# Optimization experiments

Hardware: AMD Instinct MI355X
Metric: run time of the kernel (lower is better)

## Reference

```python
import jax, jax.numpy as jnp
import numpy as np

N = 100000
E = 1600000
C_IN = 32
C_OUT = 64
DIM = 3
K = 2 ** DIM  # kernel_size=2 per pseudo-dim, degree=1 => 8 kernel slots
EPS = 1e-5

_BITS = jnp.asarray(np.array([[(c >> d) & 1 for d in range(DIM)] for c in range(K)], dtype=np.float32))  # [K,DIM]


def spline_basis(edge_attr):
    # edge_attr: [E,DIM] pseudo coords in [0,1]. kernel_size=2, degree=1 =>
    # per-dim linear basis (1-u, u); product over dims gives [E,K].
    u = edge_attr[:, None, :]            # [E,1,DIM]
    b = _BITS[None, :, :]                # [1,K,DIM]
    return jnp.prod(b * u + (1.0 - b) * (1.0 - u), axis=-1)  # [E,K]


def spline_conv(x, edge_index, edge_attr, W, W_root):
    # SplineConv with aggr='mean', root_weight=True, bias=False.
    src, dst = edge_index[0], edge_index[1]
    basis = spline_basis(edge_attr)                      # [E,K]
    x_j = x[src]                                         # [E,C_in] gather
    msg = jnp.einsum('ek,ei,kio->eo', basis, x_j, W)     # [E,C_out]
    agg = jax.ops.segment_sum(msg, dst, num_segments=N)  # [N,C_out] scatter-add
    cnt = jax.ops.segment_sum(jnp.ones((msg.shape[0],), msg.dtype), dst, num_segments=N)
    agg = agg / jnp.maximum(cnt, 1.0)[:, None]           # mean aggregation
    return agg + x @ W_root


def batch_norm(x, gamma, beta):
    mu = jnp.mean(x, axis=0)
    var = jnp.var(x, axis=0)
    return (x - mu) * jax.lax.rsqrt(var + EPS) * gamma + beta


def setup_inputs() -> dict:
    key = jax.random.key(0)
    ks = jax.random.split(key, 12)
    x = jax.random.normal(ks[0], (N, C_IN), jnp.float32)
    edge_index = jax.random.randint(ks[1], (2, E), 0, N, jnp.int32)
    edge_attr = jax.random.uniform(ks[2], (E, DIM), jnp.float32)
    s1 = 1.0 / np.sqrt(C_IN)
    s2 = 1.0 / np.sqrt(C_OUT)
    return {
        'x': x,
        'edge_index': edge_index,
        'edge_attr': edge_attr,
        'W1': jax.random.normal(ks[3], (K, C_IN, C_OUT), jnp.float32) * s1,
        'root1': jax.random.normal(ks[4], (C_IN, C_OUT), jnp.float32) * s1,
        'g1': jnp.ones((C_OUT,), jnp.float32),
        'b1': jnp.zeros((C_OUT,), jnp.float32),
        'W2': jax.random.normal(ks[5], (K, C_OUT, C_OUT), jnp.float32) * s2,
        'root2': jax.random.normal(ks[6], (C_OUT, C_OUT), jnp.float32) * s2,
        'g2': jnp.ones((C_OUT,), jnp.float32),
        'b2': jnp.zeros((C_OUT,), jnp.float32),
        'W_skip': jax.random.normal(ks[7], (C_IN, C_OUT), jnp.float32) * s1,
        'g_skip': jnp.ones((C_OUT,), jnp.float32),
        'b_skip': jnp.zeros((C_OUT,), jnp.float32),
    }


def reference(x, edge_index, edge_attr, W1, root1, g1, b1, W2, root2, g2, b2, W_skip, g_skip, b_skip):
    # ConvBlock: SplineConv -> BN -> elu
    h = spline_conv(x, edge_index, edge_attr, W1, root1)
    h = jax.nn.elu(batch_norm(h, g1, b1))
    # ConvBlockWithSkip: SplineConv -> BN; Linear skip -> BN; elu(sum)
    skip = batch_norm(x @ W_skip, g_skip, b_skip)
    h2 = batch_norm(spline_conv(h, edge_index, edge_attr, W2, root2), g2, b2)
    return jax.nn.elu(h2 + skip)
```

## Files before the change

kernel.cpp:

```cpp
#include <hip/hip_runtime.h>
#include <cstdint>

#define BN_EPS 1e-5f

typedef __attribute__((ext_vector_type(8))) short bf16x8;
typedef __attribute__((ext_vector_type(4))) float f32x4;
typedef __attribute__((ext_vector_type(2))) float f32x2;
typedef unsigned int uint32;
typedef unsigned short u16;

__device__ inline u16 f2bf(float f) {
  unsigned int b = __float_as_uint(f);
  b += 0x7FFFu + ((b >> 16) & 1u);
  return (u16)(b >> 16);
}
__device__ inline float bf2f(u16 u) { return __uint_as_float((unsigned int)u << 16); }

__global__ __launch_bounds__(256) void prep(const float* __restrict__ W1,
                                            const float* __restrict__ root1,
                                            const float* __restrict__ Wskip,
                                            const float* __restrict__ W2,
                                            const float* __restrict__ root2,
                                            u16* __restrict__ B1t, u16* __restrict__ B2t,
                                            const float* __restrict__ x,
                                            u16* __restrict__ xbf, int total8) {
  int idx = blockIdx.x * 256 + threadIdx.x;
  if (idx < 128 * 288) {
    int n = idx / 288, a = idx % 288;
    float v;
    if (a < 256) {
      int i = a >> 3, k = a & 7;
      v = (n < 64) ? W1[k * 2048 + i * 64 + n] : 0.f;
    } else {
      int i = a - 256;
      v = (n < 64) ? root1[i * 64 + n] : Wskip[i * 64 + (n - 64)];
    }
    B1t[idx] = f2bf(v);
  } else if (idx < 128 * 288 + 64 * 576) {
    int j = idx - 128 * 288;
    int n = j / 576, a = j % 576;
    float v;
    if (a < 512) {
      int i = a >> 3, k = a & 7;
      v = W2[k * 4096 + i * 64 + n];
    } else {
      v = root2[(a - 512) * 64 + n];
    }
    B2t[j] = f2bf(v);
  }
  if (idx < total8) {
    const float4* xp = (const float4*)x;
    float4 a = xp[2 * idx], b = xp[2 * idx + 1];
    union { u16 s[8]; uint4 u; } p;
    p.s[0] = f2bf(a.x); p.s[1] = f2bf(a.y); p.s[2] = f2bf(a.z); p.s[3] = f2bf(a.w);
    p.s[4] = f2bf(b.x); p.s[5] = f2bf(b.y); p.s[6] = f2bf(b.z); p.s[7] = f2bf(b.w);
    ((uint4*)xbf)[idx] = p.u;
  }
}

__global__ void hist_dst(const int* __restrict__ ei, int E, int* __restrict__ indeg,
                         int* __restrict__ rank) {
  int e = blockIdx.x * 256 + threadIdx.x;
  if (e >= E) return;
  rank[e] = atomicAdd(&indeg[ei[E + e]], 1);
}

__global__ __launch_bounds__(1024) void scan_block(const int* __restrict__ in,
                                                   int* __restrict__ part,
                                                   int* __restrict__ bsum, int N) {
  __shared__ int tmp[1024];
  int i = blockIdx.x * 1024 + threadIdx.x;
  int v = (i < N) ? in[i] : 0;
  tmp[threadIdx.x] = v;
  __syncthreads();
  for (int ofs = 1; ofs < 1024; ofs <<= 1) {
    int t = (threadIdx.x >= (unsigned)ofs) ? tmp[threadIdx.x - ofs] : 0;
    __syncthreads();
    tmp[threadIdx.x] += t;
    __syncthreads();
  }
  if (i < N) part[i] = tmp[threadIdx.x] - v;
  if (threadIdx.x == 1023) bsum[blockIdx.x] = tmp[1023];
}

__global__ __launch_bounds__(1024) void scan_top(int* __restrict__ bsum, int nb) {
  __shared__ int tmp[1024];
  int v = (threadIdx.x < (unsigned)nb) ? bsum[threadIdx.x] : 0;
  tmp[threadIdx.x] = v;
  __syncthreads();
  for (int ofs = 1; ofs < 1024; ofs <<= 1) {
    int t = (threadIdx.x >= (unsigned)ofs) ? tmp[threadIdx.x - ofs] : 0;
    __syncthreads();
    tmp[threadIdx.x] += t;
    __syncthreads();
  }
  if (threadIdx.x < (unsigned)nb) bsum[threadIdx.x] = tmp[threadIdx.x] - v;
}

__global__ void scan_add(const int* __restrict__ part, const int* __restrict__ bsum,
                         int* __restrict__ rowptr, int N, int E) {
  int i = blockIdx.x * 256 + threadIdx.x;
  if (i < N) rowptr[i] = part[i] + bsum[i >> 10];
  if (i == 0) rowptr[N] = E;
}

__global__ __launch_bounds__(256) void edge_scatter(const int* __restrict__ ei,
                                                    const float* __restrict__ attr,
                                                    const int* __restrict__ rowptr,
                                                    const int* __restrict__ rank, int E,
                                                    uint4* __restrict__ emeta) {
  int e = blockIdx.x * 256 + threadIdx.x;
  if (e >= E) return;
  int src = ei[e], dst = ei[E + e];
  union { _Float16 h[2]; uint32 u; } y, z;
  y.h[0] = (_Float16)attr[3 * e + 0];
  y.h[1] = (_Float16)attr[3 * e + 1];
  z.h[0] = (_Float16)attr[3 * e + 2];
  z.h[1] = (_Float16)0.f;
  int pos = rowptr[dst] + rank[e];
  emeta[pos] = make_uint4((uint32)src, y.u, z.u, 0u);
}

template <int PC, bool F8>
__device__ inline void sc_gather(const void* __restrict__ tab, int src, int p, float* xf) {
  if (F8) {
    u16 us = ((const u16*)tab)[(size_t)src * 32 + p];
    f32x2 a = __builtin_amdgcn_cvt_pk_f32_fp8((int)us, false);
    xf[0] = a.x;
    xf[1] = a.y;
  } else if (PC == 1) {
    xf[0] = bf2f(((const u16*)tab)[(size_t)src * 32 + p]);
  } else {
    uint32 u = *(const uint32*)((const u16*)tab + (size_t)src * 64 + 2 * p);
    xf[0] = __uint_as_float(u << 16);
    xf[1] = __uint_as_float(u & 0xFFFF0000u);
  }
}

template <int PC>
__device__ inline void sc_fma(float* acc, uint4 m, const float* xf) {
  union { uint32 u; _Float16 h[2]; } cy, cz;
  cy.u = m.y;
  cz.u = m.z;
  float u0 = (float)cy.h[0], u1 = (float)cy.h[1], u2 = (float)cz.h[0];
  float p0 = 1.f - u0, p1 = 1.f - u1, p2 = 1.f - u2;
  float w00 = p1 * p2, w10 = u1 * p2, w01 = p1 * u2, w11 = u1 * u2;
  float w[8] = {p0 * w00, u0 * w00, p0 * w10, u0 * w10,
                p0 * w01, u0 * w01, p0 * w11, u0 * w11};
#pragma unroll
  for (int k = 0; k < 8; k++) {
#pragma unroll
    for (int c = 0; c < PC; c++) acc[k * PC + c] += w[k] * xf[c];
  }
}

template <int PC, bool F8>
__global__ __launch_bounds__(256) void msg_accum(const void* __restrict__ tab,
                                                 const int* __restrict__ rowptr,
                                                 const uint4* __restrict__ emeta,
                                                 int n0, int n1, u16* __restrict__ T) {
  const int tid = threadIdx.x;
  const int lane = tid & 63;
  const int wv = tid >> 6;
  const int nwaves = gridDim.x * 4;
  const int p = lane & 31;
  const int eh = lane >> 5;

  for (int n = n0 + blockIdx.x * 4 + wv; n < n1; n += nwaves) {
    const int e0 = __builtin_amdgcn_readfirstlane(rowptr[n]);
    const int e1 = __builtin_amdgcn_readfirstlane(rowptr[n + 1]);
    float acc[8 * PC];
#pragma unroll
    for (int j = 0; j < 8 * PC; j++) acc[j] = 0.f;

    int e = e0;
    for (; e + 4 <= e1; e += 4) {
      uint4 a = emeta[e + eh];
      uint4 b = emeta[e + 2 + eh];
      float xa[PC], xb[PC];
      sc_gather<PC, F8>(tab, (int)a.x, p, xa);
      sc_gather<PC, F8>(tab, (int)b.x, p, xb);
      sc_fma<PC>(acc, a, xa);
      sc_fma<PC>(acc, b, xb);
    }
    for (; e < e1; e += 2) {
      int ee = e + eh;
      bool act = ee < e1;
      if (!act) ee = e;
      uint4 m = emeta[ee];
      float xv[PC];
      sc_gather<PC, F8>(tab, (int)m.x, p, xv);
      if (!act) {
#pragma unroll
        for (int c = 0; c < PC; c++) xv[c] = 0.f;
      }
      sc_fma<PC>(acc, m, xv);
    }

#pragma unroll
    for (int j = 0; j < 8 * PC; j++) acc[j] += __shfl_xor(acc[j], 32);

    float inv = 1.f / fmaxf((float)(e1 - e0), 1.f);
    if (eh == 0) {
      u16* rowp = T + (size_t)(n - n0) * (256 * PC);
#pragma unroll
      for (int c = 0; c < PC; c++) {
        union { u16 s[8]; uint4 u; } pk;
#pragma unroll
        for (int k = 0; k < 8; k++) pk.s[k] = f2bf(acc[k * PC + c] * inv);
        *(uint4*)(rowp + ((size_t)(PC * p + c)) * 8) = pk.u;
      }
    }
  }
}

template <int KT, int KX, int NC>
__global__ __launch_bounds__(256, 3) void gemm_agg(const u16* __restrict__ T,
                                                   const u16* __restrict__ X,
                                                   const u16* __restrict__ Bt,
                                                   u16* __restrict__ O1, u16* __restrict__ O2,
                                                   int rowOff, int rows,
                                                   double* __restrict__ sums) {
  const int K = KT + KX;
  const int tid = threadIdx.x;
  const int lane = tid & 63;
  const int wv = tid >> 6;
  const int rowbase = blockIdx.x * 64 + wv * 16;
  const int m = lane & 15;
  const int quad = lane >> 4;
  const int k0 = quad * 8;

  __shared__ float slds[4][NC][2];

  int ar = rowbase + m;
  if (ar > rows - 1) ar = rows - 1;

  bf16x8 afrag[K / 32];
#pragma unroll
  for (int f = 0; f < K / 32; f++) {
    if (f * 32 < KT)
      afrag[f] = *(const bf16x8*)(T + (size_t)ar * KT + f * 32 + k0);
    else
      afrag[f] = *(const bf16x8*)(X + (size_t)(rowOff + ar) * KX + (f * 32 - KT) + k0);
  }

  for (int col0 = 0; col0 < NC; col0 += 32) {
    f32x4 acc0 = {0.f, 0.f, 0.f, 0.f};
    f32x4 acc1 = {0.f, 0.f, 0.f, 0.f};
#pragma unroll
    for (int f = 0; f < K / 32; f++) {
      bf16x8 b0 = *(const bf16x8*)(Bt + (size_t)(col0 + m) * K + f * 32 + k0);
      bf16x8 b1 = *(const bf16x8*)(Bt + (size_t)(col0 + 16 + m) * K + f * 32 + k0);
      acc0 = __builtin_amdgcn_mfma_f32_16x16x32_bf16(afrag[f], b0, acc0, 0, 0, 0);
      acc1 = __builtin_amdgcn_mfma_f32_16x16x32_bf16(afrag[f], b1, acc1, 0, 0, 0);
    }
#pragma unroll
    for (int half = 0; half < 2; half++) {
      const f32x4& acc = half ? acc1 : acc0;
      const int col = col0 + half * 16 + m;
      float s1 = 0.f, s2 = 0.f;
#pragma unroll
      for (int r = 0; r < 4; r++) {
        int gr = rowbase + quad * 4 + r;
        if (gr < rows) {
          size_t g = (size_t)(rowOff + gr);
          u16 vq = f2bf(acc[r]);
          float v = bf2f(vq);
          s1 += v;
          s2 += v * v;
          if (NC == 64 || col < 64) O1[g * 64 + col] = vq;
          else O2[g * 64 + (col - 64)] = vq;
        }
      }
      s1 += __shfl_xor(s1, 16); s1 += __shfl_xor(s1, 32);
      s2 += __shfl_xor(s2, 16); s2 += __shfl_xor(s2, 32);
      if (lane < 16) { slds[wv][col][0] = s1; slds[wv][col][1] = s2; }
    }
  }
  __syncthreads();
  if (tid < NC * 2) {
    int col = tid >> 1, which = tid & 1;
    float v = slds[0][col][which] + slds[1][col][which] + slds[2][col][which] +
              slds[3][col][which];
    int slot = ((NC > 64 && col >= 64) ? 128 : 0) + which * 64 + (col & 63);
    atomicAdd(&sums[slot], (double)v);
  }
}

__global__ void bn_finalize2(const double* __restrict__ sums, const float* __restrict__ gA,
                             const float* __restrict__ bA, const float* __restrict__ gB,
                             const float* __restrict__ bB, float* __restrict__ scales, int N) {
  int t = threadIdx.x;
  int set = t >> 6, ch = t & 63;
  if (set == 1 && gB == nullptr) return;
  const float* g = set ? gB : gA;
  const float* b = set ? bB : bA;
  double mean = sums[set * 128 + ch] / (double)N;
  double var = sums[set * 128 + 64 + ch] / (double)N - mean * mean;
  double inv = 1.0 / sqrt(var + (double)BN_EPS);
  float sc = (float)((double)g[ch] * inv);
  scales[set * 128 + ch] = sc;
  scales[set * 128 + 64 + ch] = b[ch] - (float)mean * sc;
}

__global__ __launch_bounds__(256) void bn_elu_inplace(u16* __restrict__ h,
                                                      u16* __restrict__ h8,
                                                      const float* __restrict__ sc,
                                                      int total2) {
  int idx = blockIdx.x * 256 + threadIdx.x;
  if (idx >= total2) return;
  int ch = (idx * 2) & 63;
  uint32 u = ((const uint32*)h)[idx];
  float v0 = __uint_as_float(u << 16);
  float v1 = __uint_as_float(u & 0xFFFF0000u);
  v0 = v0 * sc[ch] + sc[64 + ch];
  v1 = v1 * sc[ch + 1] + sc[64 + ch + 1];
  v0 = v0 > 0.f ? v0 : expm1f(v0);
  v1 = v1 > 0.f ? v1 : expm1f(v1);
  ((uint32*)h)[idx] = ((uint32)f2bf(v1) << 16) | (uint32)f2bf(v0);
  int p8 = __builtin_amdgcn_cvt_pk_fp8_f32(v0, v1, 0, false);
  h8[idx] = (u16)(p8 & 0xFFFF);
}

__global__ __launch_bounds__(256) void final_k(const u16* __restrict__ h2pre,
                                               const u16* __restrict__ skip,
                                               const float* __restrict__ sc2,
                                               const float* __restrict__ scS,
                                               float* __restrict__ out, int total) {
  int idx = blockIdx.x * 256 + threadIdx.x;
  if (idx >= total) return;
  int ch = idx & 63;
  float h2 = bf2f(h2pre[idx]) * sc2[ch] + sc2[64 + ch];
  float s = bf2f(skip[idx]) * scS[ch] + scS[64 + ch];
  float v = h2 + s;
  out[idx] = v > 0.f ? v : expm1f(v);
}

extern "C" void kernel_launch(void* const* d_in, const int* in_sizes, int n_in,
                              void* d_out, int out_size, void* d_ws, size_t ws_size,
                              hipStream_t stream) {
  const float* x     = (const float*)d_in[0];
  const int*   ei    = (const int*)d_in[1];
  const float* attr  = (const float*)d_in[2];
  const float* W1    = (const float*)d_in[3];
  const float* root1 = (const float*)d_in[4];
  const float* g1    = (const float*)d_in[5];
  const float* b1    = (const float*)d_in[6];
  const float* W2    = (const float*)d_in[7];
  const float* root2 = (const float*)d_in[8];
  const float* g2    = (const float*)d_in[9];
  const float* b2    = (const float*)d_in[10];
  const float* Wskip = (const float*)d_in[11];
  const float* gS    = (const float*)d_in[12];
  const float* bS    = (const float*)d_in[13];
  const int N = in_sizes[0] / 32;
  const int E = in_sizes[1] / 2;
  const int Nh = (N + 1) / 2;
  float* out = (float*)d_out;

  char* ws = (char*)d_ws;
  size_t off = 0;
  auto alloc = [&](size_t bytes) {
    void* p = ws + off;
    off = (off + bytes + 255) & ~(size_t)255;
    return p;
  };
  u16* B1t = (u16*)alloc(128 * 288 * 2);
  u16* B2t = (u16*)alloc(64 * 576 * 2);
  double* sums = (double*)alloc(6 * 64 * 8);
  float* scales = (float*)alloc(6 * 64 * 4);
  int* indeg = (int*)alloc((size_t)N * 4);
  int* rowptr = (int*)alloc(((size_t)N + 1) * 4);
  int* part = (int*)alloc((size_t)N * 4);
  int* bsum = (int*)alloc(1024 * 4);
  int* rank = (int*)alloc((size_t)E * 4);
  uint4* emeta = (uint4*)alloc((size_t)E * 16);
  u16* xbf = (u16*)alloc((size_t)N * 32 * 2);
  u16* h8 = (u16*)alloc((size_t)N * 64);
  u16* T = (u16*)alloc((size_t)(N + 2) * 256 * 2);
  u16* h1 = (u16*)alloc((size_t)N * 64 * 2);
  u16* skip = (u16*)alloc((size_t)N * 64 * 2);
  u16* h2 = (u16*)alloc((size_t)N * 64 * 2);
  if (off > ws_size) return;

  hipMemsetAsync(indeg, 0, (size_t)N * 4, stream);
  hipMemsetAsync(sums, 0, 6 * 64 * 8, stream);

  const int eblocks = (E + 255) / 256;
  const int nb = (N + 1023) / 1024;
  prep<<<(N * 4 + 255) / 256, 256, 0, stream>>>(W1, root1, Wskip, W2, root2, B1t, B2t,
                                                x, xbf, N * 4);
  hist_dst<<<eblocks, 256, 0, stream>>>(ei, E, indeg, rank);
  scan_block<<<nb, 1024, 0, stream>>>(indeg, part, bsum, N);
  scan_top<<<1, 1024, 0, stream>>>(bsum, nb);
  scan_add<<<(N + 255) / 256, 256, 0, stream>>>(part, bsum, rowptr, N, E);
  edge_scatter<<<eblocks, 256, 0, stream>>>(ei, attr, rowptr, rank, E, emeta);

  msg_accum<1, false><<<2048, 256, 0, stream>>>(xbf, rowptr, emeta, 0, N, T);
  gemm_agg<256, 32, 128><<<(N + 63) / 64, 256, 0, stream>>>(T, xbf, B1t, h1, skip, 0, N,
                                                            sums);
  bn_finalize2<<<1, 128, 0, stream>>>(sums, g1, b1, gS, bS, scales, N);
  bn_elu_inplace<<<(N * 32 + 255) / 256, 256, 0, stream>>>(h1, h8, scales, N * 32);

  for (int cph = 0; cph < 2; cph++) {
    int r0 = cph ? Nh : 0;
    int r1 = cph ? N : Nh;
    msg_accum<2, true><<<2048, 256, 0, stream>>>(h8, rowptr, emeta, r0, r1, T);
    gemm_agg<512, 64, 64><<<(r1 - r0 + 63) / 64, 256, 0, stream>>>(T, h1, B2t, h2, nullptr,
                                                                   r0, r1 - r0,
                                                                   sums + 4 * 64);
  }
  bn_finalize2<<<1, 64, 0, stream>>>(sums + 4 * 64, g2, b2, nullptr, nullptr,
                                     scales + 4 * 64, N);

  final_k<<<(N * 64 + 255) / 256, 256, 0, stream>>>(h2, skip, scales + 4 * 64,
                                                    scales + 2 * 64, out, N * 64);
}
```

Baseline: 590.4 us.

## Widen per-lane channel work in message gather and stage GEMM weights in LDS

The message-accumulation kernel now assigns 16 lanes per edge with 2 or 4 channels each, so each wave processes four edges at once and issues wider 4-byte gathers. Partial sums are reduced with an extra cross-lane shuffle. The aggregation GEMM copies half of the transposed weight matrix into padded shared memory per pass instead of reading B fragments from global memory. This raises register pressure in the accumulator (up to 32 floats per lane) and adds block barriers in the GEMM.

```diff
diff --git a/kernel.cpp b/kernel.cpp
--- a/kernel.cpp
+++ b/kernel.cpp
@@ -124,14 +124,12 @@
 template <int PC, bool F8>
 __device__ inline void sc_gather(const void* __restrict__ tab, int src, int p, float* xf) {
   if (F8) {
-    u16 us = ((const u16*)tab)[(size_t)src * 32 + p];
-    f32x2 a = __builtin_amdgcn_cvt_pk_f32_fp8((int)us, false);
-    xf[0] = a.x;
-    xf[1] = a.y;
-  } else if (PC == 1) {
-    xf[0] = bf2f(((const u16*)tab)[(size_t)src * 32 + p]);
+    uint32 u = *(const uint32*)((const char*)tab + (size_t)src * 64 + 4 * p);
+    f32x2 a = __builtin_amdgcn_cvt_pk_f32_fp8((int)u, false);
+    f32x2 b = __builtin_amdgcn_cvt_pk_f32_fp8((int)u, true);
+    xf[0] = a.x; xf[1] = a.y; xf[2] = b.x; xf[3] = b.y;
   } else {
-    uint32 u = *(const uint32*)((const u16*)tab + (size_t)src * 64 + 2 * p);
+    uint32 u = *(const uint32*)((const u16*)tab + (size_t)src * 32 + 2 * p);
     xf[0] = __uint_as_float(u << 16);
     xf[1] = __uint_as_float(u & 0xFFFF0000u);
   }
@@ -163,8 +161,8 @@
   const int lane = tid & 63;
   const int wv = tid >> 6;
   const int nwaves = gridDim.x * 4;
-  const int p = lane & 31;
-  const int eh = lane >> 5;
+  const int p = lane & 15;
+  const int eh = lane >> 4;
 
   for (int n = n0 + blockIdx.x * 4 + wv; n < n1; n += nwaves) {
     const int e0 = __builtin_amdgcn_readfirstlane(rowptr[n]);
@@ -174,16 +172,16 @@
     for (int j = 0; j < 8 * PC; j++) acc[j] = 0.f;
 
     int e = e0;
-    for (; e + 4 <= e1; e += 4) {
+    for (; e + 8 <= e1; e += 8) {
       uint4 a = emeta[e + eh];
-      uint4 b = emeta[e + 2 + eh];
+      uint4 b = emeta[e + 4 + eh];
       float xa[PC], xb[PC];
       sc_gather<PC, F8>(tab, (int)a.x, p, xa);
       sc_gather<PC, F8>(tab, (int)b.x, p, xb);
       sc_fma<PC>(acc, a, xa);
       sc_fma<PC>(acc, b, xb);
     }
-    for (; e < e1; e += 2) {
+    for (; e < e1; e += 4) {
       int ee = e + eh;
       bool act = ee < e1;
       if (!act) ee = e;
@@ -198,11 +196,14 @@
     }
 
 #pragma unroll
-    for (int j = 0; j < 8 * PC; j++) acc[j] += __shfl_xor(acc[j], 32);
+    for (int j = 0; j < 8 * PC; j++) {
+      acc[j] += __shfl_xor(acc[j], 16);
+      acc[j] += __shfl_xor(acc[j], 32);
+    }
 
     float inv = 1.f / fmaxf((float)(e1 - e0), 1.f);
     if (eh == 0) {
-      u16* rowp = T + (size_t)(n - n0) * (256 * PC);
+      u16* rowp = T + (size_t)(n - n0) * (128 * PC);
 #pragma unroll
       for (int c = 0; c < PC; c++) {
         union { u16 s[8]; uint4 u; } pk;
@@ -222,6 +223,8 @@
                                                    int rowOff, int rows,
                                                    double* __restrict__ sums) {
   const int K = KT + KX;
+  const int KP = K + 8;
+  const int NCH = NC / 2;
   const int tid = threadIdx.x;
   const int lane = tid & 63;
   const int wv = tid >> 6;
@@ -230,6 +233,7 @@
   const int quad = lane >> 4;
   const int k0 = quad * 8;
 
+  __shared__ u16 bs[NCH * (KT + KX + 8)];
   __shared__ float slds[4][NC][2];
 
   int ar = rowbase + m;
@@ -244,37 +248,48 @@
       afrag[f] = *(const bf16x8*)(X + (size_t)(rowOff + ar) * KX + (f * 32 - KT) + k0);
   }
 
-  for (int col0 = 0; col0 < NC; col0 += 32) {
-    f32x4 acc0 = {0.f, 0.f, 0.f, 0.f};
-    f32x4 acc1 = {0.f, 0.f, 0.f, 0.f};
-#pragma unroll
-    for (int f = 0; f < K / 32; f++) {
-      bf16x8 b0 = *(const bf16x8*)(Bt + (size_t)(col0 + m) * K + f * 32 + k0);
-      bf16x8 b1 = *(const bf16x8*)(Bt + (size_t)(col0 + 16 + m) * K + f * 32 + k0);
-      acc0 = __builtin_amdgcn_mfma_f32_16x16x32_bf16(afrag[f], b0, acc0, 0, 0, 0);
-      acc1 = __builtin_amdgcn_mfma_f32_16x16x32_bf16(afrag[f], b1, acc1, 0, 0, 0);
-    }
-#pragma unroll
-    for (int half = 0; half < 2; half++) {
-      const f32x4& acc = half ? acc1 : acc0;
-      const int col = col0 + half * 16 + m;
-      float s1 = 0.f, s2 = 0.f;
-#pragma unroll
-      for (int r = 0; r < 4; r++) {
-        int gr = rowbase + quad * 4 + r;
-        if (gr < rows) {
-          size_t g = (size_t)(rowOff + gr);
-          u16 vq = f2bf(acc[r]);
-          float v = bf2f(vq);
-          s1 += v;
-          s2 += v * v;
-          if (NC == 64 || col < 64) O1[g * 64 + col] = vq;
-          else O2[g * 64 + (col - 64)] = vq;
+  for (int halfc = 0; halfc < 2; halfc++) {
+    __syncthreads();
+    for (int i = tid; i < NCH * (K / 8); i += 256) {
+      int col = i / (K / 8);
+      int kk = (i % (K / 8)) * 8;
+      *(uint4*)(bs + col * KP + kk) =
+          *(const uint4*)(Bt + (size_t)(halfc * NCH + col) * K + kk);
+    }
+    __syncthreads();
+
+    for (int col0 = 0; col0 < NCH; col0 += 32) {
+      f32x4 acc0 = {0.f, 0.f, 0.f, 0.f};
+      f32x4 acc1 = {0.f, 0.f, 0.f, 0.f};
+#pragma unroll
+      for (int f = 0; f < K / 32; f++) {
+        bf16x8 b0 = *(const bf16x8*)(bs + (col0 + m) * KP + f * 32 + k0);
+        bf16x8 b1 = *(const bf16x8*)(bs + (col0 + 16 + m) * KP + f * 32 + k0);
+        acc0 = __builtin_amdgcn_mfma_f32_16x16x32_bf16(afrag[f], b0, acc0, 0, 0, 0);
+        acc1 = __builtin_amdgcn_mfma_f32_16x16x32_bf16(afrag[f], b1, acc1, 0, 0, 0);
+      }
+#pragma unroll
+      for (int half = 0; half < 2; half++) {
+        const f32x4& acc = half ? acc1 : acc0;
+        const int col = halfc * NCH + col0 + half * 16 + m;
+        float s1 = 0.f, s2 = 0.f;
+#pragma unroll
+        for (int r = 0; r < 4; r++) {
+          int gr = rowbase + quad * 4 + r;
+          if (gr < rows) {
+            size_t g = (size_t)(rowOff + gr);
+            u16 vq = f2bf(acc[r]);
+            float v = bf2f(vq);
+            s1 += v;
+            s2 += v * v;
+            if (NC == 64 || col < 64) O1[g * 64 + col] = vq;
+            else O2[g * 64 + (col - 64)] = vq;
+          }
         }
+        s1 += __shfl_xor(s1, 16); s1 += __shfl_xor(s1, 32);
+        s2 += __shfl_xor(s2, 16); s2 += __shfl_xor(s2, 32);
+        if (lane < 16) { slds[wv][col][0] = s1; slds[wv][col][1] = s2; }
       }
-      s1 += __shfl_xor(s1, 16); s1 += __shfl_xor(s1, 32);
-      s2 += __shfl_xor(s2, 16); s2 += __shfl_xor(s2, 32);
-      if (lane < 16) { slds[wv][col][0] = s1; slds[wv][col][1] = s2; }
     }
   }
   __syncthreads();
@@ -396,7 +411,7 @@
   scan_add<<<(N + 255) / 256, 256, 0, stream>>>(part, bsum, rowptr, N, E);
   edge_scatter<<<eblocks, 256, 0, stream>>>(ei, attr, rowptr, rank, E, emeta);
 
-  msg_accum<1, false><<<2048, 256, 0, stream>>>(xbf, rowptr, emeta, 0, N, T);
+  msg_accum<2, false><<<2048, 256, 0, stream>>>(xbf, rowptr, emeta, 0, N, T);
   gemm_agg<256, 32, 128><<<(N + 63) / 64, 256, 0, stream>>>(T, xbf, B1t, h1, skip, 0, N,
                                                             sums);
   bn_finalize2<<<1, 128, 0, stream>>>(sums, g1, b1, gS, bS, scales, N);
@@ -405,7 +420,7 @@
   for (int cph = 0; cph < 2; cph++) {
     int r0 = cph ? Nh : 0;
     int r1 = cph ? N : Nh;
-    msg_accum<2, true><<<2048, 256, 0, stream>>>(h8, rowptr, emeta, r0, r1, T);
+    msg_accum<4, true><<<2048, 256, 0, stream>>>(h8, rowptr, emeta, r0, r1, T);
     gemm_agg<512, 64, 64><<<(r1 - r0 + 63) / 64, 256, 0, stream>>>(T, h1, B2t, h2, nullptr,
                                                                    r0, r1 - r0,
                                                                    sums + 4 * 64);
```

After: 561.7 us. -4.9%, faster.
